# Kernel optimization log

Hardware: AMD Instinct MI355X
Metric: run time of the kernel (lower is better)

## Reference

```python
import jax, jax.numpy as jnp
import numpy as np

N, IN_DIM, OUT_DIM, HEADS = 8192, 256, 256, 2
C = OUT_DIM // HEADS  # per-head channel dim (concat=True)
ALPHA = 0.2
NEG = -9e15


def setup_inputs() -> dict:
    key = jax.random.key(0)
    ks = jax.random.split(key, 9)
    h = jax.random.normal(ks[0], (N, IN_DIM), dtype=jnp.float32)
    adj = jax.random.randint(ks[1], (N, N), 0, 2, dtype=jnp.int32)
    # torch nn.Linear weights are [out, in]; xavier-like scale
    def xav(k, shape):
        fan_in, fan_out = shape[1], shape[0]
        s = 1.414 * np.sqrt(6.0 / (fan_in + fan_out))
        return jax.random.uniform(k, shape, jnp.float32, -s, s)
    W1 = xav(ks[2], (HEADS * C, IN_DIM))
    W2 = xav(ks[3], (HEADS * C, IN_DIM))
    W3 = xav(ks[4], (HEADS * C, IN_DIM))
    b1 = jnp.zeros((HEADS * C,), jnp.float32)
    b2 = jnp.zeros((HEADS * C,), jnp.float32)
    b3 = jnp.zeros((HEADS * C,), jnp.float32)
    sa = 1.414 * np.sqrt(6.0 / (HEADS + 2 * C))
    a = jax.random.uniform(ks[5], (HEADS, 2 * C), jnp.float32, -sa, sa)
    return {"h": h, "adj": adj, "W1": W1, "b1": b1, "W2": W2, "b2": b2,
            "W3": W3, "b3": b3, "a": a}


def reference(h, adj, W1, b1, W2, b2, W3, b3, a):
    n = h.shape[0]
    W1h = (h @ W1.T + b1).reshape(n, HEADS, C)  # [N,H,C]
    W2h = (h @ W2.T + b2).reshape(n, HEADS, C)
    W3h = (h @ W3.T + b3).reshape(n, HEADS, C)
    # eij = a . [W1h_i || W2h_j] decomposes into per-node scores
    a1, a2 = a[:, :C], a[:, C:]
    s1 = jnp.einsum('nhc,hc->nh', W1h, a1)  # [N,H]
    s2 = jnp.einsum('nhc,hc->nh', W2h, a2)  # [N,H]
    e = jax.nn.leaky_relu(s1[:, None, :] + s2[None, :, :], ALPHA)  # [N,N,H]
    e = jnp.where(adj[:, :, None] == 1, e, NEG)
    att = jax.nn.softmax(e, axis=1)  # softmax over source dim j (dim=1)
    # dropout is identity in eval mode (training=False)
    h_prime = jnp.einsum('ijh,jhc->ihc', att, W3h)  # [N,H,C]
    return h_prime.reshape(n, HEADS * C)
```

## Files before the change

kernel.cpp:

```cpp
#include <hip/hip_runtime.h>
#include <hip/hip_bf16.h>

#define NN 8192
#define LOG2E 1.44269504088896f
#define S_SPLIT 8
#define JC 1024
#define NT 32

typedef __attribute__((ext_vector_type(8))) short short8;
typedef __attribute__((ext_vector_type(4))) float f32x4;

static __device__ __forceinline__ float bf2f(unsigned short u) {
    union { unsigned int i; float f; } v; v.i = ((unsigned int)u) << 16; return v.f;
}
static __device__ __forceinline__ unsigned short f2bf(float f) {
    union { float f; unsigned int i; } v; v.f = f;
    unsigned int lsb = (v.i >> 16) & 1u;
    v.i += 0x7fffu + lsb;
    return (unsigned short)(v.i >> 16);
}
static __device__ __forceinline__ unsigned int cvtpk(float lo, float hi) {
    unsigned int r;
    asm("v_cvt_pk_bf16_f32 %0, %1, %2" : "=v"(r) : "v"(lo), "v"(hi));
    return r;
}
static __device__ __forceinline__ float fexp2(float x) { return __builtin_amdgcn_exp2f(x); }

static __device__ __forceinline__ void cvt8(const float* __restrict__ p, short8& hi, short8& lo) {
    float4 u = *(const float4*)p;
    float4 v = *(const float4*)(p + 4);
    float f[8] = {u.x, u.y, u.z, u.w, v.x, v.y, v.z, v.w};
#pragma unroll
    for (int j = 0; j < 8; ++j) {
        unsigned short hb = f2bf(f[j]);
        hi[j] = (short)hb;
        lo[j] = (short)f2bf(f[j] - bf2f(hb));
    }
}

__global__ __launch_bounds__(256) void pack_kernel(const int* __restrict__ adj,
                                                   unsigned int* __restrict__ abits,
                                                   const float* __restrict__ W3,
                                                   unsigned short* __restrict__ w3hi,
                                                   unsigned short* __restrict__ w3lo) {
    int b = blockIdx.x;
    if (b < 8192) {
        int w = b * 256 + threadIdx.x;
        const int* src = adj + (size_t)w * 32;
        unsigned int bits = 0;
#pragma unroll
        for (int k = 0; k < 8; ++k) {
            int4 v = *(const int4*)(src + k * 4);
            bits |= (unsigned int)(v.x & 1) << (k * 4 + 0);
            bits |= (unsigned int)(v.y & 1) << (k * 4 + 1);
            bits |= (unsigned int)(v.z & 1) << (k * 4 + 2);
            bits |= (unsigned int)(v.w & 1) << (k * 4 + 3);
        }
        abits[w] = bits;
    } else {
        int i = (b - 8192) * 256 + threadIdx.x;
        float f = W3[i];
        unsigned short hb = f2bf(f);
        w3hi[i] = hb;
        w3lo[i] = f2bf(f - bf2f(hb));
    }
}

__global__ void prep_partial(const float* __restrict__ W1, const float* __restrict__ W2,
                             const float* __restrict__ a,
                             float* __restrict__ v1p, float* __restrict__ v2p) {
    int b = blockIdx.x;
    int t = threadIdx.x;
    int hh = t >> 8, k = t & 255;
    int c0 = (b & 7) * 16;
    const float* W = (b < 8) ? W1 : W2;
    int aoff = (b < 8) ? 0 : 128;
    float acc = 0.f;
    for (int c = c0; c < c0 + 16; ++c)
        acc += W[(size_t)(hh * 128 + c) * 256 + k] * a[hh * 256 + aoff + c];
    ((b < 8) ? v1p : v2p)[(b & 7) * 512 + t] = acc;
}

__global__ void prep_reduce(const float* __restrict__ b1, const float* __restrict__ b2,
                            const float* __restrict__ a,
                            const float* __restrict__ v1p, const float* __restrict__ v2p,
                            float* __restrict__ v1, float* __restrict__ v2, float* __restrict__ bd) {
    int t = threadIdx.x;
    float a1 = 0.f, a2 = 0.f;
    for (int b = 0; b < 8; ++b) { a1 += v1p[b * 512 + t]; a2 += v2p[b * 512 + t]; }
    v1[t] = a1;
    v2[t] = a2;
    int g = t >> 7;
    int hh = g >> 1, which = g & 1, c = t & 127;
    float prod = which ? b2[hh * 128 + c] * a[hh * 256 + 128 + c]
                       : b1[hh * 128 + c] * a[hh * 256 + c];
#pragma unroll
    for (int off = 1; off < 64; off <<= 1) prod += __shfl_xor(prod, off);
    __shared__ float ws[8];
    if ((t & 63) == 0) ws[t >> 6] = prod;
    __syncthreads();
    if (t < 4) bd[t] = ws[2 * t] + ws[2 * t + 1];
}

__global__ __launch_bounds__(256) void s_kernel(const float* __restrict__ hmat,
                         const float* __restrict__ v1, const float* __restrict__ v2,
                         const float* __restrict__ bd,
                         float* __restrict__ s1o, float* __restrict__ s2o) {
    int w = threadIdx.x >> 6, l = threadIdx.x & 63;
    int n = blockIdx.x * 4 + w;
    float4 hv  = *(const float4*)(hmat + (size_t)n * 256 + l * 4);
    float4 va0 = *(const float4*)(v1 + l * 4);
    float4 va1 = *(const float4*)(v1 + 256 + l * 4);
    float4 vb0 = *(const float4*)(v2 + l * 4);
    float4 vb1 = *(const float4*)(v2 + 256 + l * 4);
    float s10 = hv.x*va0.x + hv.y*va0.y + hv.z*va0.z + hv.w*va0.w;
    float s11 = hv.x*va1.x + hv.y*va1.y + hv.z*va1.z + hv.w*va1.w;
    float s20 = hv.x*vb0.x + hv.y*vb0.y + hv.z*vb0.z + hv.w*vb0.w;
    float s21 = hv.x*vb1.x + hv.y*vb1.y + hv.z*vb1.z + hv.w*vb1.w;
#pragma unroll
    for (int off = 1; off < 64; off <<= 1) {
        s10 += __shfl_xor(s10, off);
        s11 += __shfl_xor(s11, off);
        s20 += __shfl_xor(s20, off);
        s21 += __shfl_xor(s21, off);
    }
    if (l == 0) {
        s1o[n*2 + 0] = (s10 + bd[0]) * LOG2E;
        s1o[n*2 + 1] = (s11 + bd[2]) * LOG2E;
        s2o[n]       = (s20 + bd[1]) * LOG2E;
        s2o[NN + n]  = (s21 + bd[3]) * LOG2E;
    }
}

__global__ __launch_bounds__(256) void w3_kernel(const float* __restrict__ hmat,
                                                 const unsigned short* __restrict__ w3hi,
                                                 const unsigned short* __restrict__ w3lo,
                                                 const float* __restrict__ b3,
                                                 unsigned short* __restrict__ w3b) {
    int tid = threadIdx.x;
    int w = tid >> 6, l = tid & 63;
    int m = l & 15, kq = l >> 4;
    int n0 = (blockIdx.x * 2 + (w & 1)) * 16;
    int c0 = (w >> 1) * 8;
    f32x4 acc[8];
#pragma unroll
    for (int ct = 0; ct < 8; ++ct) acc[ct] = (f32x4){0.f, 0.f, 0.f, 0.f};
    for (int k0 = 0; k0 < 256; k0 += 32) {
        short8 ahi, alo;
        cvt8(hmat + (size_t)(n0 + m) * 256 + k0 + kq * 8, ahi, alo);
#pragma unroll
        for (int ct = 0; ct < 8; ++ct) {
            int c = (c0 + ct) * 16 + m;
            short8 bhi = *(const short8*)&w3hi[(size_t)c * 256 + k0 + kq * 8];
            short8 blo = *(const short8*)&w3lo[(size_t)c * 256 + k0 + kq * 8];
            acc[ct] = __builtin_amdgcn_mfma_f32_16x16x32_bf16(ahi, bhi, acc[ct], 0, 0, 0);
            acc[ct] = __builtin_amdgcn_mfma_f32_16x16x32_bf16(alo, bhi, acc[ct], 0, 0, 0);
            acc[ct] = __builtin_amdgcn_mfma_f32_16x16x32_bf16(ahi, blo, acc[ct], 0, 0, 0);
        }
    }
#pragma unroll
    for (int ct = 0; ct < 8; ++ct) {
        int c = (c0 + ct) * 16 + m;
        float bias = b3[c];
#pragma unroll
        for (int e = 0; e < 4; ++e) {
            int n = n0 + kq * 4 + e;
            size_t idx = ((size_t)(n >> 5) * 16 + (c >> 4)) * 512 + (size_t)((((n >> 3) & 3) * 16 + m) * 8 + (n & 7));
            w3b[idx] = f2bf(acc[ct][e] + bias);
        }
    }
}

__global__ __launch_bounds__(256, 4) void attn_fused(
        const unsigned int* __restrict__ abits, const float* __restrict__ s1a,
        const float* __restrict__ s2h, const unsigned short* __restrict__ w3b,
        unsigned short* __restrict__ pacc, float* __restrict__ pden)
{
    __shared__ unsigned short Pt[2][2][64][32];
    __shared__ float s2t[2][JC];
    __shared__ unsigned int abt[64][32];

    const int tid = threadIdx.x;
    const int ln = tid & 63;
    const int m = ln & 15, kq = ln >> 4;
    const int cg = tid >> 6;
    const int hw = cg >> 1;
    const int r = tid >> 2, oc = tid & 3;
    const int i0 = blockIdx.x * 64;
    const int sidx = blockIdx.y;
    const int j0 = sidx * JC;
    const int sw = kq ^ ((m >> 1) & 3);

    const float s1r0 = s1a[(i0 + r) * 2 + 0];
    const float s1r1 = s1a[(i0 + r) * 2 + 1];
    unsigned short* ptw = &Pt[0][0][0][0] + r * 32 + ((oc ^ ((r >> 1) & 3)) << 3);
    const unsigned short* pta = &Pt[0][0][0][0] + hw * 2048 + m * 32 + (sw << 3);
    const unsigned short* w3p = w3b + ((size_t)(j0 >> 5) * 16 + cg * 4) * 512 + ln * 8;

    f32x4 acc[4][4];
#pragma unroll
    for (int rt = 0; rt < 4; ++rt)
#pragma unroll
        for (int f = 0; f < 4; ++f) acc[rt][f] = (f32x4){0.f, 0.f, 0.f, 0.f};
    float d0 = 0.f, d1 = 0.f;

    for (int x = tid; x < 2 * JC; x += 256) {
        int h = x >> 10, j = x & (JC - 1);
        s2t[h][j] = s2h[(size_t)h * NN + j0 + j];
    }
    for (int x = tid; x < 64 * 32; x += 256) {
        int rr = x >> 5, tt = x & 31;
        abt[rr][tt] = abits[(size_t)(i0 + rr) * 256 + (j0 >> 5) + tt];
    }
    __syncthreads();

    for (int t = 0; t < NT; ++t) {
        const int buf = t & 1;
        const unsigned short* bp = w3p + (size_t)t * 8192;
        short8 bf0 = *(const short8*)(bp);
        short8 bf1 = *(const short8*)(bp + 512);
        short8 bf2 = *(const short8*)(bp + 1024);
        short8 bf3 = *(const short8*)(bp + 1536);
        {
            unsigned int bits = abt[r][t] >> (oc * 8);
            uint4 w0, w1;
            {
                float4 sv0 = *(const float4*)&s2t[0][t * 32 + oc * 8];
                float4 sv1 = *(const float4*)&s2t[1][t * 32 + oc * 8];
                float x0, q0, q1, q2, q3, u0, u1, u2, u3;
                x0 = s1r0 + sv0.x; x0 = fmaxf(x0, 0.2f * x0); q0 = (bits & 1u) ? fexp2(x0) : 0.f;
                x0 = s1r0 + sv0.y; x0 = fmaxf(x0, 0.2f * x0); q1 = (bits & 2u) ? fexp2(x0) : 0.f;
                x0 = s1r0 + sv0.z; x0 = fmaxf(x0, 0.2f * x0); q2 = (bits & 4u) ? fexp2(x0) : 0.f;
                x0 = s1r0 + sv0.w; x0 = fmaxf(x0, 0.2f * x0); q3 = (bits & 8u) ? fexp2(x0) : 0.f;
                x0 = s1r1 + sv1.x; x0 = fmaxf(x0, 0.2f * x0); u0 = (bits & 1u) ? fexp2(x0) : 0.f;
                x0 = s1r1 + sv1.y; x0 = fmaxf(x0, 0.2f * x0); u1 = (bits & 2u) ? fexp2(x0) : 0.f;
                x0 = s1r1 + sv1.z; x0 = fmaxf(x0, 0.2f * x0); u2 = (bits & 4u) ? fexp2(x0) : 0.f;
                x0 = s1r1 + sv1.w; x0 = fmaxf(x0, 0.2f * x0); u3 = (bits & 8u) ? fexp2(x0) : 0.f;
                d0 += (q0 + q1) + (q2 + q3);
                d1 += (u0 + u1) + (u2 + u3);
                w0.x = cvtpk(q0, q1); w0.y = cvtpk(q2, q3);
                w1.x = cvtpk(u0, u1); w1.y = cvtpk(u2, u3);
            }
            {
                float4 sv0 = *(const float4*)&s2t[0][t * 32 + oc * 8 + 4];
                float4 sv1 = *(const float4*)&s2t[1][t * 32 + oc * 8 + 4];
                float x0, q0, q1, q2, q3, u0, u1, u2, u3;
                x0 = s1r0 + sv0.x; x0 = fmaxf(x0, 0.2f * x0); q0 = (bits & 16u)  ? fexp2(x0) : 0.f;
                x0 = s1r0 + sv0.y; x0 = fmaxf(x0, 0.2f * x0); q1 = (bits & 32u)  ? fexp2(x0) : 0.f;
                x0 = s1r0 + sv0.z; x0 = fmaxf(x0, 0.2f * x0); q2 = (bits & 64u)  ? fexp2(x0) : 0.f;
                x0 = s1r0 + sv0.w; x0 = fmaxf(x0, 0.2f * x0); q3 = (bits & 128u) ? fexp2(x0) : 0.f;
                x0 = s1r1 + sv1.x; x0 = fmaxf(x0, 0.2f * x0); u0 = (bits & 16u)  ? fexp2(x0) : 0.f;
                x0 = s1r1 + sv1.y; x0 = fmaxf(x0, 0.2f * x0); u1 = (bits & 32u)  ? fexp2(x0) : 0.f;
                x0 = s1r1 + sv1.z; x0 = fmaxf(x0, 0.2f * x0); u2 = (bits & 64u)  ? fexp2(x0) : 0.f;
                x0 = s1r1 + sv1.w; x0 = fmaxf(x0, 0.2f * x0); u3 = (bits & 128u) ? fexp2(x0) : 0.f;
                d0 += (q0 + q1) + (q2 + q3);
                d1 += (u0 + u1) + (u2 + u3);
                w0.z = cvtpk(q0, q1); w0.w = cvtpk(q2, q3);
                w1.z = cvtpk(u0, u1); w1.w = cvtpk(u2, u3);
            }
            unsigned short* pw = ptw + buf * 4096;
            *(uint4*)pw = w0;
            *(uint4*)(pw + 2048) = w1;
        }
        __syncthreads();
        {
            const unsigned short* pa = pta + buf * 4096;
#pragma unroll
            for (int rt = 0; rt < 4; ++rt) {
                short8 a = *(const short8*)(pa + rt * 512);
                acc[rt][0] = __builtin_amdgcn_mfma_f32_16x16x32_bf16(a, bf0, acc[rt][0], 0, 0, 0);
                acc[rt][1] = __builtin_amdgcn_mfma_f32_16x16x32_bf16(a, bf1, acc[rt][1], 0, 0, 0);
                acc[rt][2] = __builtin_amdgcn_mfma_f32_16x16x32_bf16(a, bf2, acc[rt][2], 0, 0, 0);
                acc[rt][3] = __builtin_amdgcn_mfma_f32_16x16x32_bf16(a, bf3, acc[rt][3], 0, 0, 0);
            }
        }
    }

    d0 += __shfl_xor(d0, 1); d0 += __shfl_xor(d0, 2);
    d1 += __shfl_xor(d1, 1); d1 += __shfl_xor(d1, 2);
    if (oc == 0) {
        size_t base = ((size_t)sidx * NN + i0 + r) * 2;
        pden[base + 0] = d0;
        pden[base + 1] = d1;
    }
    size_t pb_ = (size_t)sidx * NN * 256;
#pragma unroll
    for (int rt = 0; rt < 4; ++rt)
#pragma unroll
        for (int e = 0; e < 4; ++e) {
            int row = i0 + rt * 16 + kq * 4 + e;
#pragma unroll
            for (int f = 0; f < 4; ++f) {
                int col = cg * 64 + f * 16 + m;
                __builtin_nontemporal_store(f2bf(acc[rt][f][e]), &pacc[pb_ + (size_t)row * 256 + col]);
            }
        }
}

__global__ void combine_kernel(const unsigned short* __restrict__ pacc, const float* __restrict__ pden,
                               float* __restrict__ out) {
    size_t idx = ((size_t)blockIdx.x * 256 + threadIdx.x) * 8;
    int i = (int)(idx >> 8);
    int c = (int)(idx & 255);
    int hh = c >> 7;
    float acc[8];
#pragma unroll
    for (int e = 0; e < 8; ++e) acc[e] = 0.f;
    float den = 0.f;
    for (int s = 0; s < S_SPLIT; ++s) {
        uint4 v = *(const uint4*)&pacc[(size_t)s * NN * 256 + idx];
        unsigned int uu[4] = {v.x, v.y, v.z, v.w};
#pragma unroll
        for (int q = 0; q < 4; ++q) {
            acc[2*q]   += bf2f((unsigned short)(uu[q] & 0xffff));
            acc[2*q+1] += bf2f((unsigned short)(uu[q] >> 16));
        }
        den += pden[((size_t)s * NN + i) * 2 + hh];
    }
    float r = 1.f / den;
    float4 o0 = {acc[0]*r, acc[1]*r, acc[2]*r, acc[3]*r};
    float4 o1 = {acc[4]*r, acc[5]*r, acc[6]*r, acc[7]*r};
    *(float4*)&out[idx] = o0;
    *(float4*)&out[idx + 4] = o1;
}

extern "C" void kernel_launch(void* const* d_in, const int* in_sizes, int n_in,
                              void* d_out, int out_size, void* d_ws, size_t ws_size,
                              hipStream_t stream) {
    const float* hmat = (const float*)d_in[0];
    const int*   adj  = (const int*)d_in[1];
    const float* W1   = (const float*)d_in[2];
    const float* b1   = (const float*)d_in[3];
    const float* W2   = (const float*)d_in[4];
    const float* b2   = (const float*)d_in[5];
    const float* W3   = (const float*)d_in[6];
    const float* b3   = (const float*)d_in[7];
    const float* a    = (const float*)d_in[8];
    float* out = (float*)d_out;

    char* p = (char*)d_ws;
    float* v1   = (float*)p; p += 2048;
    float* v2   = (float*)p; p += 2048;
    float* bd   = (float*)p; p += 256;
    float* s1   = (float*)p; p += (size_t)NN * 2 * sizeof(float);
    float* s2h  = (float*)p; p += (size_t)NN * 2 * sizeof(float);
    float* v1p  = (float*)p; p += 8 * 512 * sizeof(float);
    float* v2p  = (float*)p; p += 8 * 512 * sizeof(float);
    unsigned short* w3hi = (unsigned short*)p; p += 65536 * 2;
    unsigned short* w3lo = (unsigned short*)p; p += 65536 * 2;
    unsigned short* w3b  = (unsigned short*)p; p += (size_t)NN * 256 * 2;
    unsigned int* abits  = (unsigned int*)p;   p += (size_t)NN * 256 * sizeof(unsigned int);
    float* pden = (float*)p; p += (size_t)S_SPLIT * NN * 2 * sizeof(float);
    unsigned short* pacc = (unsigned short*)p;

    pack_kernel<<<8192 + 256, 256, 0, stream>>>(adj, abits, W3, w3hi, w3lo);
    prep_partial<<<16, 512, 0, stream>>>(W1, W2, a, v1p, v2p);
    prep_reduce<<<1, 512, 0, stream>>>(b1, b2, a, v1p, v2p, v1, v2, bd);
    s_kernel<<<NN / 4, 256, 0, stream>>>(hmat, v1, v2, bd, s1, s2h);
    w3_kernel<<<256, 256, 0, stream>>>(hmat, w3hi, w3lo, b3, w3b);
    attn_fused<<<dim3(NN / 64, S_SPLIT), 256, 0, stream>>>(abits, s1, s2h, w3b, pacc, pden);
    combine_kernel<<<(NN * 256) / (256 * 8), 256, 0, stream>>>(pacc, pden, out);
}
```

Baseline: 153.2 us.

## Factor leaky-relu exponentials into per-node products and stream adjacency bits from global

Uses exp2(lrelu(s1+s2)) = exp2(s1)*exp2(s2) when the sum is positive, else exp2(0.2*s1)*exp2(0.2*s2). Per-source exponentials are precomputed in s_kernel and per-row factors in registers, so the inner loop does compares and multiplies instead of one exp per edge. Adjacency words are now read per thread from global with one-step prefetch instead of being staged in LDS, and the occupancy hint rises from 4 to 5 blocks. Risks include overflow or underflow of the separate exponent factors, rounding differences at the sign boundary, and more global loads in the loop.

After: 465.1 us. 3.04x slower.

```diff
diff --git a/kernel.cpp b/kernel.cpp
--- a/kernel.cpp
+++ b/kernel.cpp
@@ -105,7 +105,8 @@
 __global__ __launch_bounds__(256) void s_kernel(const float* __restrict__ hmat,
                          const float* __restrict__ v1, const float* __restrict__ v2,
                          const float* __restrict__ bd,
-                         float* __restrict__ s1o, float* __restrict__ s2o) {
+                         float* __restrict__ s1o, float* __restrict__ e2g,
+                         float* __restrict__ e2wg) {
     int w = threadIdx.x >> 6, l = threadIdx.x & 63;
     int n = blockIdx.x * 4 + w;
     float4 hv  = *(const float4*)(hmat + (size_t)n * 256 + l * 4);
@@ -127,8 +128,12 @@
     if (l == 0) {
         s1o[n*2 + 0] = (s10 + bd[0]) * LOG2E;
         s1o[n*2 + 1] = (s11 + bd[2]) * LOG2E;
-        s2o[n]       = (s20 + bd[1]) * LOG2E;
-        s2o[NN + n]  = (s21 + bd[3]) * LOG2E;
+        float s20L = (s20 + bd[1]) * LOG2E;
+        float s21L = (s21 + bd[3]) * LOG2E;
+        e2g[n]        = fexp2(s20L);
+        e2g[NN + n]   = fexp2(s21L);
+        e2wg[n]       = fexp2(0.2f * s20L);
+        e2wg[NN + n]  = fexp2(0.2f * s21L);
     }
 }
 
@@ -171,14 +176,14 @@
     }
 }
 
-__global__ __launch_bounds__(256, 4) void attn_fused(
+__global__ __launch_bounds__(256, 5) void attn_fused(
         const unsigned int* __restrict__ abits, const float* __restrict__ s1a,
-        const float* __restrict__ s2h, const unsigned short* __restrict__ w3b,
+        const float* __restrict__ e2g, const float* __restrict__ e2wg,
+        const unsigned short* __restrict__ w3b,
         unsigned short* __restrict__ pacc, float* __restrict__ pden)
 {
     __shared__ unsigned short Pt[2][2][64][32];
-    __shared__ float s2t[2][JC];
-    __shared__ unsigned int abt[64][32];
+    __shared__ float et[4][JC];
 
     const int tid = threadIdx.x;
     const int ln = tid & 63;
@@ -191,11 +196,16 @@
     const int j0 = sidx * JC;
     const int sw = kq ^ ((m >> 1) & 3);
 
-    const float s1r0 = s1a[(i0 + r) * 2 + 0];
-    const float s1r1 = s1a[(i0 + r) * 2 + 1];
+    const float s1L0 = s1a[(i0 + r) * 2 + 0];
+    const float s1L1 = s1a[(i0 + r) * 2 + 1];
+    const float E10 = fexp2(s1L0),        E11 = fexp2(s1L1);
+    const float W10 = fexp2(0.2f * s1L0), W11 = fexp2(0.2f * s1L1);
+    const float R10 = fexp2(-s1L0),       R11 = fexp2(-s1L1);
+
     unsigned short* ptw = &Pt[0][0][0][0] + r * 32 + ((oc ^ ((r >> 1) & 3)) << 3);
     const unsigned short* pta = &Pt[0][0][0][0] + hw * 2048 + m * 32 + (sw << 3);
     const unsigned short* w3p = w3b + ((size_t)(j0 >> 5) * 16 + cg * 4) * 512 + ln * 8;
+    const unsigned int* abR = abits + (size_t)(i0 + r) * 256 + (j0 >> 5);
 
     f32x4 acc[4][4];
 #pragma unroll
@@ -204,14 +214,12 @@
         for (int f = 0; f < 4; ++f) acc[rt][f] = (f32x4){0.f, 0.f, 0.f, 0.f};
     float d0 = 0.f, d1 = 0.f;
 
-    for (int x = tid; x < 2 * JC; x += 256) {
-        int h = x >> 10, j = x & (JC - 1);
-        s2t[h][j] = s2h[(size_t)h * NN + j0 + j];
-    }
-    for (int x = tid; x < 64 * 32; x += 256) {
-        int rr = x >> 5, tt = x & 31;
-        abt[rr][tt] = abits[(size_t)(i0 + rr) * 256 + (j0 >> 5) + tt];
-    }
+    for (int x = tid; x < 4 * JC; x += 256) {
+        int pl = x >> 10, j = x & (JC - 1);
+        const float* src = (pl < 2) ? (e2g + (size_t)pl * NN) : (e2wg + (size_t)(pl - 2) * NN);
+        et[pl][j] = src[j0 + j];
+    }
+    unsigned int bitsC = abR[0];
     __syncthreads();
 
     for (int t = 0; t < NT; ++t) {
@@ -221,46 +229,39 @@
         short8 bf1 = *(const short8*)(bp + 512);
         short8 bf2 = *(const short8*)(bp + 1024);
         short8 bf3 = *(const short8*)(bp + 1536);
+        unsigned int bitsN = abR[(t + 1 < NT) ? t + 1 : t];
         {
-            unsigned int bits = abt[r][t] >> (oc * 8);
-            uint4 w0, w1;
-            {
-                float4 sv0 = *(const float4*)&s2t[0][t * 32 + oc * 8];
-                float4 sv1 = *(const float4*)&s2t[1][t * 32 + oc * 8];
-                float x0, q0, q1, q2, q3, u0, u1, u2, u3;
-                x0 = s1r0 + sv0.x; x0 = fmaxf(x0, 0.2f * x0); q0 = (bits & 1u) ? fexp2(x0) : 0.f;
-                x0 = s1r0 + sv0.y; x0 = fmaxf(x0, 0.2f * x0); q1 = (bits & 2u) ? fexp2(x0) : 0.f;
-                x0 = s1r0 + sv0.z; x0 = fmaxf(x0, 0.2f * x0); q2 = (bits & 4u) ? fexp2(x0) : 0.f;
-                x0 = s1r0 + sv0.w; x0 = fmaxf(x0, 0.2f * x0); q3 = (bits & 8u) ? fexp2(x0) : 0.f;
-                x0 = s1r1 + sv1.x; x0 = fmaxf(x0, 0.2f * x0); u0 = (bits & 1u) ? fexp2(x0) : 0.f;
-                x0 = s1r1 + sv1.y; x0 = fmaxf(x0, 0.2f * x0); u1 = (bits & 2u) ? fexp2(x0) : 0.f;
-                x0 = s1r1 + sv1.z; x0 = fmaxf(x0, 0.2f * x0); u2 = (bits & 4u) ? fexp2(x0) : 0.f;
-                x0 = s1r1 + sv1.w; x0 = fmaxf(x0, 0.2f * x0); u3 = (bits & 8u) ? fexp2(x0) : 0.f;
-                d0 += (q0 + q1) + (q2 + q3);
-                d1 += (u0 + u1) + (u2 + u3);
-                w0.x = cvtpk(q0, q1); w0.y = cvtpk(q2, q3);
-                w1.x = cvtpk(u0, u1); w1.y = cvtpk(u2, u3);
+            unsigned int bits = bitsC >> (oc * 8);
+            float4 eA0 = *(const float4*)&et[0][t * 32 + oc * 8];
+            float4 eB0 = *(const float4*)&et[0][t * 32 + oc * 8 + 4];
+            float4 eA1 = *(const float4*)&et[1][t * 32 + oc * 8];
+            float4 eB1 = *(const float4*)&et[1][t * 32 + oc * 8 + 4];
+            float4 wA0 = *(const float4*)&et[2][t * 32 + oc * 8];
+            float4 wB0 = *(const float4*)&et[2][t * 32 + oc * 8 + 4];
+            float4 wA1 = *(const float4*)&et[3][t * 32 + oc * 8];
+            float4 wB1 = *(const float4*)&et[3][t * 32 + oc * 8 + 4];
+            float e0[8] = {eA0.x, eA0.y, eA0.z, eA0.w, eB0.x, eB0.y, eB0.z, eB0.w};
+            float e1[8] = {eA1.x, eA1.y, eA1.z, eA1.w, eB1.x, eB1.y, eB1.z, eB1.w};
+            float w0_[8] = {wA0.x, wA0.y, wA0.z, wA0.w, wB0.x, wB0.y, wB0.z, wB0.w};
+            float w1_[8] = {wA1.x, wA1.y, wA1.z, wA1.w, wB1.x, wB1.y, wB1.z, wB1.w};
+            float p0[8], p1[8];
+#pragma unroll
+            for (int k = 0; k < 8; ++k) {
+                bool on = (bits >> k) & 1u;
+                bool pos0 = e0[k] > R10;
+                bool pos1 = e1[k] > R11;
+                float f0 = (pos0 ? e0[k] : w0_[k]) * (pos0 ? E10 : W10);
+                float f1 = (pos1 ? e1[k] : w1_[k]) * (pos1 ? E11 : W11);
+                p0[k] = on ? f0 : 0.f;
+                p1[k] = on ? f1 : 0.f;
             }
-            {
-                float4 sv0 = *(const float4*)&s2t[0][t * 32 + oc * 8 + 4];
-                float4 sv1 = *(const float4*)&s2t[1][t * 32 + oc * 8 + 4];
-                float x0, q0, q1, q2, q3, u0, u1, u2, u3;
-                x0 = s1r0 + sv0.x; x0 = fmaxf(x0, 0.2f * x0); q0 = (bits & 16u)  ? fexp2(x0) : 0.f;
-                x0 = s1r0 + sv0.y; x0 = fmaxf(x0, 0.2f * x0); q1 = (bits & 32u)  ? fexp2(x0) : 0.f;
-                x0 = s1r0 + sv0.z; x0 = fmaxf(x0, 0.2f * x0); q2 = (bits & 64u)  ? fexp2(x0) : 0.f;
-                x0 = s1r0 + sv0.w; x0 = fmaxf(x0, 0.2f * x0); q3 = (bits & 128u) ? fexp2(x0) : 0.f;
-                x0 = s1r1 + sv1.x; x0 = fmaxf(x0, 0.2f * x0); u0 = (bits & 16u)  ? fexp2(x0) : 0.f;
-                x0 = s1r1 + sv1.y; x0 = fmaxf(x0, 0.2f * x0); u1 = (bits & 32u)  ? fexp2(x0) : 0.f;
-                x0 = s1r1 + sv1.z; x0 = fmaxf(x0, 0.2f * x0); u2 = (bits & 64u)  ? fexp2(x0) : 0.f;
-                x0 = s1r1 + sv1.w; x0 = fmaxf(x0, 0.2f * x0); u3 = (bits & 128u) ? fexp2(x0) : 0.f;
-                d0 += (q0 + q1) + (q2 + q3);
-                d1 += (u0 + u1) + (u2 + u3);
-                w0.z = cvtpk(q0, q1); w0.w = cvtpk(q2, q3);
-                w1.z = cvtpk(u0, u1); w1.w = cvtpk(u2, u3);
-            }
+#pragma unroll
+            for (int k = 0; k < 8; ++k) { d0 += p0[k]; d1 += p1[k]; }
+            uint4 wv0 = {cvtpk(p0[0], p0[1]), cvtpk(p0[2], p0[3]), cvtpk(p0[4], p0[5]), cvtpk(p0[6], p0[7])};
+            uint4 wv1 = {cvtpk(p1[0], p1[1]), cvtpk(p1[2], p1[3]), cvtpk(p1[4], p1[5]), cvtpk(p1[6], p1[7])};
             unsigned short* pw = ptw + buf * 4096;
-            *(uint4*)pw = w0;
-            *(uint4*)(pw + 2048) = w1;
+            *(uint4*)pw = wv0;
+            *(uint4*)(pw + 2048) = wv1;
         }
         __syncthreads();
         {
@@ -274,6 +275,7 @@
                 acc[rt][3] = __builtin_amdgcn_mfma_f32_16x16x32_bf16(a, bf3, acc[rt][3], 0, 0, 0);
             }
         }
+        bitsC = bitsN;
     }
 
     d0 += __shfl_xor(d0, 1); d0 += __shfl_xor(d0, 2);
@@ -343,7 +345,8 @@
     float* v2   = (float*)p; p += 2048;
     float* bd   = (float*)p; p += 256;
     float* s1   = (float*)p; p += (size_t)NN * 2 * sizeof(float);
-    float* s2h  = (float*)p; p += (size_t)NN * 2 * sizeof(float);
+    float* e2g  = (float*)p; p += (size_t)NN * 2 * sizeof(float);
+    float* e2wg = (float*)p; p += (size_t)NN * 2 * sizeof(float);
     float* v1p  = (float*)p; p += 8 * 512 * sizeof(float);
     float* v2p  = (float*)p; p += 8 * 512 * sizeof(float);
     unsigned short* w3hi = (unsigned short*)p; p += 65536 * 2;
@@ -356,8 +359,8 @@
     pack_kernel<<<8192 + 256, 256, 0, stream>>>(adj, abits, W3, w3hi, w3lo);
     prep_partial<<<16, 512, 0, stream>>>(W1, W2, a, v1p, v2p);
     prep_reduce<<<1, 512, 0, stream>>>(b1, b2, a, v1p, v2p, v1, v2, bd);
-    s_kernel<<<NN / 4, 256, 0, stream>>>(hmat, v1, v2, bd, s1, s2h);
+    s_kernel<<<NN / 4, 256, 0, stream>>>(hmat, v1, v2, bd, s1, e2g, e2wg);
     w3_kernel<<<256, 256, 0, stream>>>(hmat, w3hi, w3lo, b3, w3b);
-    attn_fused<<<dim3(NN / 64, S_SPLIT), 256, 0, stream>>>(abits, s1, s2h, w3b, pacc, pden);
+    attn_fused<<<dim3(NN / 64, S_SPLIT), 256, 0, stream>>>(abits, s1, e2g, e2wg, w3b, pacc, pden);
     combine_kernel<<<(NN * 256) / (256 * 8), 256, 0, stream>>>(pacc, pden, out);
 }
```
